# Kernel optimization log

Hardware: AMD Instinct MI355X
Metric: run time of the kernel (lower is better)

The kernel has to match this reference:

```python
import jax, jax.numpy as jnp
import numpy as np

NUM_HEADS = 16
ROPE_THETA = 1000.0


def _rope(x, cos, sin):
    # x: [B, H, T, d_k]; cos/sin: [T, d_k//2]
    xp = x.reshape(x.shape[:-1] + (x.shape[-1] // 2, 2))
    xe, xo = xp[..., 0], xp[..., 1]
    c = cos[None, None, :, :]
    s = sin[None, None, :, :]
    re = xe * c - xo * s
    ro = xe * s + xo * c
    return jnp.stack((re, ro), axis=-1).reshape(x.shape)


def setup_inputs() -> dict:
    key = jax.random.key(0)
    ks = jax.random.split(key, 5)
    B, T, D = 2, 2048, 1024
    std = 2.0 / (D + D)
    return {
        "x": jax.random.normal(ks[0], (B, T, D), dtype=jnp.float32),
        "wq": jax.random.normal(ks[1], (D, D), dtype=jnp.float32) * std,
        "wk": jax.random.normal(ks[2], (D, D), dtype=jnp.float32) * std,
        "wv": jax.random.normal(ks[3], (D, D), dtype=jnp.float32) * std,
        "wo": jax.random.normal(ks[4], (D, D), dtype=jnp.float32) * std,
    }


def reference(x, wq, wk, wv, wo):
    B, T, D = x.shape
    H = NUM_HEADS
    dk = D // H

    def proj(w):
        # Linear stores weight as [out, in]: '... in, out in -> ... out'
        y = jnp.einsum('btd,ed->bte', x, w)
        return y.reshape(B, T, H, dk).transpose(0, 2, 1, 3)  # [B,H,T,dk]

    q = proj(wq)
    k = proj(wk)
    v = proj(wv)

    # RoPE tables
    pos = jnp.arange(T, dtype=jnp.float32)[:, None]
    kidx = jnp.arange(dk // 2, dtype=jnp.float32)
    inv_freq = ROPE_THETA ** (-2.0 * kidx / dk)
    ang = pos * inv_freq[None, :]
    cos, sin = jnp.cos(ang), jnp.sin(ang)

    q = _rope(q, cos, sin)
    k = _rope(k, cos, sin)

    scores = jnp.einsum('bhnd,bhmd->bhnm', q, k) / jnp.sqrt(jnp.asarray(dk, x.dtype))
    causal = jnp.tril(jnp.ones((T, T), dtype=bool))
    scores = jnp.where(causal[None, None], scores, -jnp.inf)
    attn = jax.nn.softmax(scores, axis=-1)
    head = jnp.einsum('bhnm,bhmd->bhnd', attn, v)  # [B,H,T,dk]

    concat = head.transpose(0, 2, 1, 3).reshape(B, T, D)
    return jnp.einsum('btd,ed->bte', concat, wo)
```

## Files before the change

kernel.cpp:

```cpp
#include <hip/hip_runtime.h>
#include <hip/hip_bf16.h>

typedef __hip_bfloat16 bf16;
typedef __attribute__((ext_vector_type(8))) short bf16x8;
typedef __attribute__((ext_vector_type(4))) float f32x4;

#define T_SEQ 2048
#define NHEADS 16
#define DK 64
#define DMODEL 1024

__device__ inline void load_lds16(const void* g, void* l) {
    __builtin_amdgcn_global_load_lds((const __attribute__((address_space(1))) void*)g,
                                     (__attribute__((address_space(3))) void*)l, 16, 0, 0);
}

__global__ void cvt_all(const float* __restrict__ x,  const float* __restrict__ wq,
                        const float* __restrict__ wk, const float* __restrict__ wv,
                        const float* __restrict__ wo, bf16* __restrict__ xb,
                        bf16* __restrict__ wqkvb, bf16* __restrict__ wob) {
    int i = blockIdx.x * blockDim.x + threadIdx.x;
    const float* src; bf16* dst; int off;
    if (i < (1 << 20)) { src = x; dst = xb; off = i; }
    else {
        int j = i - (1 << 20);
        int seg = j >> 18; off = j & ((1 << 18) - 1);
        src = (seg == 0) ? wq : (seg == 1) ? wk : (seg == 2) ? wv : wo;
        dst = (seg < 3) ? (wqkvb + ((size_t)seg << 20)) : wob;
    }
    float4 f = ((const float4*)src)[off];
    ushort4 o;
    o.x = __bfloat16_as_ushort(__float2bfloat16(f.x));
    o.y = __bfloat16_as_ushort(__float2bfloat16(f.y));
    o.z = __bfloat16_as_ushort(__float2bfloat16(f.z));
    o.w = __bfloat16_as_ushort(__float2bfloat16(f.w));
    ((ushort4*)dst)[off] = o;
}

__global__ __launch_bounds__(256, 4) void gemm_qkv_rope(const bf16* __restrict__ A,
                                                        const bf16* __restrict__ B,
                                                        bf16* __restrict__ qb,
                                                        bf16* __restrict__ kb,
                                                        bf16* __restrict__ vt) {
    const int K = 1024;
    __shared__ bf16 As[128 * 64];
    __shared__ bf16 Bs[128 * 64];
    const int tid  = threadIdx.x;
    const int lane = tid & 63;
    const int wave = tid >> 6;
    const int l16  = lane & 15;
    const int quad = lane >> 4;
    const int wy = wave >> 1, wx = wave & 1;
    const int brow = blockIdx.y * 128;
    const int bcol = blockIdx.x * 128;
    const int sw0 = (quad ^ (l16 & 7)) * 8;
    const int sw1 = ((4 + quad) ^ (l16 & 7)) * 8;

    f32x4 acc[4][4] = {};

    for (int k0 = 0; k0 < K; k0 += 64) {
#pragma unroll
        for (int i = 0; i < 4; ++i) {
            int j   = tid + 256 * i;
            int row = j >> 3;
            int blk = (j & 7) ^ (row & 7);
            load_lds16(A + (size_t)(brow + row) * K + k0 + blk * 8, (char*)As + j * 16);
            load_lds16(B + (size_t)(bcol + row) * K + k0 + blk * 8, (char*)Bs + j * 16);
        }
        __syncthreads();
#pragma unroll
        for (int ks = 0; ks < 2; ++ks) {
            const int sw = ks ? sw1 : sw0;
            bf16x8 af[4], bq[4];
#pragma unroll
            for (int i = 0; i < 4; ++i)
                af[i] = *(const bf16x8*)(As + (wy * 64 + i * 16 + l16) * 64 + sw);
#pragma unroll
            for (int j = 0; j < 4; ++j)
                bq[j] = *(const bf16x8*)(Bs + (wx * 64 + j * 16 + l16) * 64 + sw);
#pragma unroll
            for (int i = 0; i < 4; ++i)
#pragma unroll
                for (int j = 0; j < 4; ++j)
                    acc[i][j] = __builtin_amdgcn_mfma_f32_16x16x32_bf16(af[i], bq[j], acc[i][j], 0, 0, 0);
        }
        __syncthreads();
    }
    const int seg = bcol >> 10;
    const int hh  = ((bcol & 1023) >> 6) + wx;
    if (seg < 2) {
        bf16* dst = seg ? kb : qb;
        const float osc = seg ? 1.0f : 0.18033688011112042f;
#pragma unroll
        for (int j = 0; j < 4; ++j) {
            const int d = j * 16 + l16;
            const float inv = exp2f(-0.31143075889f * (float)(d >> 1));
#pragma unroll
            for (int i = 0; i < 4; ++i)
#pragma unroll
                for (int r = 0; r < 4; ++r) {
                    int row = brow + wy * 64 + i * 16 + quad * 4 + r;
                    int t = row & (T_SEQ - 1), bi = row >> 11;
                    float s, c;
                    __sincosf((float)t * inv, &s, &c);
                    float v = acc[i][j][r];
                    float p = __shfl_xor(v, 1);
                    float res = (l16 & 1) ? fmaf(p, s, v * c) : fmaf(-p, s, v * c);
                    dst[((size_t)(bi * NHEADS + hh) * T_SEQ + t) * DK + d] =
                        __float2bfloat16(res * osc);
                }
        }
    } else {
#pragma unroll
        for (int j = 0; j < 4; ++j) {
            const int d = j * 16 + l16;
#pragma unroll
            for (int i = 0; i < 4; ++i)
#pragma unroll
                for (int r = 0; r < 4; ++r) {
                    int row = brow + wy * 64 + i * 16 + quad * 4 + r;
                    int t = row & (T_SEQ - 1), bi = row >> 11;
                    vt[((size_t)(bi * NHEADS + hh) * DK + d) * T_SEQ + t] =
                        __float2bfloat16(acc[i][j][r]);
                }
        }
    }
}

__global__ __launch_bounds__(256, 4) void gemm_bt(const bf16* __restrict__ A,
                                                  const bf16* __restrict__ B,
                                                  float* __restrict__ C,
                                                  int M, int N, int K) {
    __shared__ bf16 As[128 * 64];
    __shared__ bf16 Bs[128 * 64];
    const int tid  = threadIdx.x;
    const int lane = tid & 63;
    const int wave = tid >> 6;
    const int l16  = lane & 15;
    const int quad = lane >> 4;
    const int wy = wave >> 1, wx = wave & 1;
    const int brow = blockIdx.y * 128;
    const int bcol = blockIdx.x * 128;
    const int sw0 = (quad ^ (l16 & 7)) * 8;
    const int sw1 = ((4 + quad) ^ (l16 & 7)) * 8;

    f32x4 acc[4][4] = {};

    for (int k0 = 0; k0 < K; k0 += 64) {
#pragma unroll
        for (int i = 0; i < 4; ++i) {
            int j   = tid + 256 * i;
            int row = j >> 3;
            int blk = (j & 7) ^ (row & 7);
            load_lds16(A + (size_t)(brow + row) * K + k0 + blk * 8, (char*)As + j * 16);
            load_lds16(B + (size_t)(bcol + row) * K + k0 + blk * 8, (char*)Bs + j * 16);
        }
        __syncthreads();
#pragma unroll
        for (int ks = 0; ks < 2; ++ks) {
            const int sw = ks ? sw1 : sw0;
            bf16x8 af[4], bq[4];
#pragma unroll
            for (int i = 0; i < 4; ++i)
                af[i] = *(const bf16x8*)(As + (wy * 64 + i * 16 + l16) * 64 + sw);
#pragma unroll
            for (int j = 0; j < 4; ++j)
                bq[j] = *(const bf16x8*)(Bs + (wx * 64 + j * 16 + l16) * 64 + sw);
#pragma unroll
            for (int i = 0; i < 4; ++i)
#pragma unroll
                for (int j = 0; j < 4; ++j)
                    acc[i][j] = __builtin_amdgcn_mfma_f32_16x16x32_bf16(af[i], bq[j], acc[i][j], 0, 0, 0);
        }
        __syncthreads();
    }
#pragma unroll
    for (int i = 0; i < 4; ++i)
#pragma unroll
        for (int j = 0; j < 4; ++j)
#pragma unroll
            for (int r = 0; r < 4; ++r) {
                int row = brow + wy * 64 + i * 16 + quad * 4 + r;
                int col = bcol + wx * 64 + j * 16 + l16;
                C[(size_t)row * N + col] = acc[i][j][r];
            }
}

__constant__ unsigned char c_sched[24] = {
    28, 61, 57, 58, 24, 53, 49, 20,
    62, 54, 50, 41, 42, 16, 45, 46,
     0,  4,  8, 12, 33, 37, 34, 38};

__global__ __launch_bounds__(256, 4) void attn_kernel(const bf16* __restrict__ qb,
                                                      const bf16* __restrict__ kb,
                                                      const bf16* __restrict__ vt,
                                                      float* __restrict__ Oacc,
                                                      float* __restrict__ Lacc,
                                                      bf16* __restrict__ conc) {
    __shared__ bf16 Ks[2][64 * 64];
    __shared__ bf16 Vs[2][64 * 64];
    __shared__ bf16 Pl[4][16 * 64];
    const int bh = blockIdx.y;
    const int b = bh >> 4, h = bh & 15;

    const int e    = c_sched[blockIdx.x];
    const int tile = e >> 2, mode = e & 3;
    const int it0  = (mode == 2) ? tile + 1 : 0;
    const int it1  = (mode == 1) ? tile : 2 * tile + 1;
    const bool partial = (mode != 0);
    const int qbase = tile << 7;

    const int tid = threadIdx.x;
    const int lane = tid & 63, wave = tid >> 6;
    const int l16 = lane & 15, quad = lane >> 4;
    const int qr0 = qbase + wave * 16;
    const int qr1 = qr0 + 64;

    const bf16* Qp = qb + (size_t)bh * T_SEQ * DK;
    const bf16* Kp = kb + (size_t)bh * T_SEQ * DK;
    const bf16* Vp = vt + (size_t)bh * DK * T_SEQ;
    char* Pw = (char*)&Pl[wave][0];

    const short one_bits = 0x3F80;
    const bf16x8 ones = {one_bits, one_bits, one_bits, one_bits,
                         one_bits, one_bits, one_bits, one_bits};

    bf16x8 qf[2][2];
#pragma unroll
    for (int s = 0; s < 2; ++s) {
        qf[0][s] = *(const bf16x8*)(Qp + (size_t)(qr0 + l16) * DK + s * 32 + quad * 8);
        qf[1][s] = *(const bf16x8*)(Qp + (size_t)(qr1 + l16) * DK + s * 32 + quad * 8);
    }

    auto stage = [&](int bb, int k0) {
        int j = tid;
#pragma unroll
        for (int i = 0; i < 2; ++i, j += 256) {
            int row = j >> 3, cbl = (j & 7) ^ ((j >> 3) & 7);
            load_lds16(Kp + (size_t)(k0 + row) * DK + cbl * 8, (char*)Ks[bb] + j * 16);
        }
        j = tid;
#pragma unroll
        for (int i = 0; i < 2; ++i, j += 256) {
            int row = j >> 3, cbl = (j & 7) ^ ((j >> 3) & 7);
            load_lds16(Vp + (size_t)row * T_SEQ + k0 + cbl * 8, (char*)Vs[bb] + j * 16);
        }
    };

    f32x4 o0[4] = {}, o1[4] = {};
    f32x4 ol0 = {}, ol1 = {};
    const int sw0 = (quad ^ (l16 & 7)) * 8;
    const int sw1 = ((4 + quad) ^ (l16 & 7)) * 8;
    const int pw_wr_base = l16 * 128 + (quad & 1) * 8;
    const int pq = quad >> 1;

    int cur = 0;
    stage(0, it0 * 64);
    for (int it = it0; it <= it1; ++it) {
        __syncthreads();
        if (it < it1) stage(cur ^ 1, (it + 1) * 64);

        const int k0 = it * 64;
        const bool skip0 = (k0 > qr0 + 15);
        const bool diag0 = (k0 + 63 > qr0) && !skip0;
        const bool diag1 = (k0 + 63 > qr1);

        f32x4 s0[4] = {}, s1[4] = {};
        __builtin_amdgcn_s_setprio(1);
#pragma unroll
        for (int nt = 0; nt < 4; ++nt) {
            bf16x8 kf0 = *(const bf16x8*)(Ks[cur] + (nt * 16 + l16) * 64 + sw0);
            bf16x8 kf1 = *(const bf16x8*)(Ks[cur] + (nt * 16 + l16) * 64 + sw1);
            if (!skip0) {
                s0[nt] = __builtin_amdgcn_mfma_f32_16x16x32_bf16(kf0, qf[0][0], s0[nt], 0, 0, 0);
                s0[nt] = __builtin_amdgcn_mfma_f32_16x16x32_bf16(kf1, qf[0][1], s0[nt], 0, 0, 0);
            }
            s1[nt] = __builtin_amdgcn_mfma_f32_16x16x32_bf16(kf0, qf[1][0], s1[nt], 0, 0, 0);
            s1[nt] = __builtin_amdgcn_mfma_f32_16x16x32_bf16(kf1, qf[1][1], s1[nt], 0, 0, 0);
        }
        __builtin_amdgcn_s_setprio(0);

        if (!skip0) {
#pragma unroll
            for (int nt = 0; nt < 4; ++nt) {
                union { bf16 hv[4]; uint2 u; } pk;
#pragma unroll
                for (int r = 0; r < 4; ++r) {
                    float v = s0[nt][r];
                    if (diag0 && (k0 + nt * 16 + quad * 4 + r > qr0 + l16)) v = -30.0f;
                    pk.hv[r] = __float2bfloat16(exp2f(v));
                }
                *(uint2*)(Pw + pw_wr_base + (((nt * 2 + pq) ^ (l16 & 7)) << 4)) = pk.u;
            }
            __builtin_amdgcn_s_setprio(1);
#pragma unroll
            for (int ks = 0; ks < 2; ++ks) {
                bf16x8 pf = *(const bf16x8*)(Pw + l16 * 128 + (((ks * 4 + quad) ^ (l16 & 7)) << 4));
                const int sw = ks ? sw1 : sw0;
                ol0 = __builtin_amdgcn_mfma_f32_16x16x32_bf16(pf, ones, ol0, 0, 0, 0);
#pragma unroll
                for (int j = 0; j < 4; ++j) {
                    bf16x8 vf = *(const bf16x8*)(Vs[cur] + (j * 16 + l16) * 64 + sw);
                    o0[j] = __builtin_amdgcn_mfma_f32_16x16x32_bf16(pf, vf, o0[j], 0, 0, 0);
                }
            }
            __builtin_amdgcn_s_setprio(0);
        }

#pragma unroll
        for (int nt = 0; nt < 4; ++nt) {
            union { bf16 hv[4]; uint2 u; } pk;
#pragma unroll
            for (int r = 0; r < 4; ++r) {
                float v = s1[nt][r];
                if (diag1 && (k0 + nt * 16 + quad * 4 + r > qr1 + l16)) v = -30.0f;
                pk.hv[r] = __float2bfloat16(exp2f(v));
            }
            *(uint2*)(Pw + pw_wr_base + (((nt * 2 + pq) ^ (l16 & 7)) << 4)) = pk.u;
        }
        __builtin_amdgcn_s_setprio(1);
#pragma unroll
        for (int ks = 0; ks < 2; ++ks) {
            bf16x8 pf = *(const bf16x8*)(Pw + l16 * 128 + (((ks * 4 + quad) ^ (l16 & 7)) << 4));
            const int sw = ks ? sw1 : sw0;
            ol1 = __builtin_amdgcn_mfma_f32_16x16x32_bf16(pf, ones, ol1, 0, 0, 0);
#pragma unroll
            for (int j = 0; j < 4; ++j) {
                bf16x8 vf = *(const bf16x8*)(Vs[cur] + (j * 16 + l16) * 64 + sw);
                o1[j] = __builtin_amdgcn_mfma_f32_16x16x32_bf16(pf, vf, o1[j], 0, 0, 0);
            }
        }
        __builtin_amdgcn_s_setprio(0);
        cur ^= 1;
    }

#pragma unroll
    for (int g = 0; g < 2; ++g) {
        const f32x4* op = g ? o1 : o0;
        const f32x4 lv = g ? ol1 : ol0;
        const int qr = g ? qr1 : qr0;
        if (!partial) {
#pragma unroll
            for (int r = 0; r < 4; ++r) {
                float inv_l = 1.0f / lv[r];
                int t = qr + quad * 4 + r;
#pragma unroll
                for (int j = 0; j < 4; ++j)
                    conc[((size_t)b * T_SEQ + t) * DMODEL + h * DK + j * 16 + l16] =
                        __float2bfloat16(op[j][r] * inv_l);
            }
        } else {
#pragma unroll
            for (int r = 0; r < 4; ++r) {
                int q = qr + quad * 4 + r;
                if (l16 == 0)
                    atomicAdd(&Lacc[(size_t)bh * 1024 + q - 1024], lv[r]);
                float* Ob = Oacc + ((size_t)bh * 1024 + q - 1024) * DK;
#pragma unroll
                for (int j = 0; j < 4; ++j)
                    atomicAdd(&Ob[j * 16 + l16], op[j][r]);
            }
        }
    }
}

__global__ void attn_finalize(const float* __restrict__ Oacc, const float* __restrict__ Lacc,
                              bf16* __restrict__ conc) {
    int i4 = blockIdx.x * blockDim.x + threadIdx.x;
    if (i4 >= (1 << 19)) return;
    int bhq = i4 >> 4;
    int d4  = i4 & 15;
    int bh = bhq >> 10, q1 = bhq & 1023;
    int b = bh >> 4, h = bh & 15;
    int q = 1024 + q1;
    float inv = 1.0f / Lacc[bhq];
    float4 o4 = ((const float4*)Oacc)[i4];
    ushort4 u;
    u.x = __bfloat16_as_ushort(__float2bfloat16(o4.x * inv));
    u.y = __bfloat16_as_ushort(__float2bfloat16(o4.y * inv));
    u.z = __bfloat16_as_ushort(__float2bfloat16(o4.z * inv));
    u.w = __bfloat16_as_ushort(__float2bfloat16(o4.w * inv));
    *(ushort4*)&conc[((size_t)(b * T_SEQ + q)) * DMODEL + h * DK + d4 * 4] = u;
}

extern "C" void kernel_launch(void* const* d_in, const int* in_sizes, int n_in,
                              void* d_out, int out_size, void* d_ws, size_t ws_size,
                              hipStream_t stream) {
    const float* x  = (const float*)d_in[0];
    const float* wq = (const float*)d_in[1];
    const float* wk = (const float*)d_in[2];
    const float* wv = (const float*)d_in[3];
    const float* wo = (const float*)d_in[4];
    float* out = (float*)d_out;

    char* ws = (char*)d_ws;
    bf16* xb    = (bf16*)(ws);
    bf16* wqkvb = (bf16*)(ws + (8ull << 20));
    bf16* wob   = (bf16*)(ws + (14ull << 20));
    bf16* qb    = (bf16*)(ws + (40ull << 20));
    bf16* kb    = (bf16*)(ws + (48ull << 20));
    bf16* vt    = (bf16*)(ws + (56ull << 20));
    bf16* conc  = (bf16*)(ws + (16ull << 20));
    float* Oacc = (float*)(ws + (24ull << 20));
    float* Lacc = (float*)(ws + (32ull << 20));

    cvt_all<<<8192, 256, 0, stream>>>(x, wq, wk, wv, wo, xb, wqkvb, wob);
    gemm_qkv_rope<<<dim3(24, 32), 256, 0, stream>>>(xb, wqkvb, qb, kb, vt);

    hipMemsetAsync(Oacc, 0, (8ull << 20) + 32 * 1024 * sizeof(float), stream);
    attn_kernel<<<dim3(24, 32), 256, 0, stream>>>(qb, kb, vt, Oacc, Lacc, conc);
    attn_finalize<<<2048, 256, 0, stream>>>(Oacc, Lacc, conc);

    gemm_bt<<<dim3(8, 32), 256, 0, stream>>>(conc, wob, out, 4096, 1024, 1024);
}
```

Before: 182.7 us.

## Rebalance causal attention work with per-block multi-segment split schedule

Replaces the fixed 24-entry tile/mode schedule with a table where each block handles up to two segments, each encoding a query tile and an arbitrary key-iteration range. More query tiles (rows 768 and up) can now be split into partial segments merged with atomics, and the accumulator buffers and finalize kernel grow to cover 1280 rows per head. The goal is to even out per-block causal work so the grid finishes together. In exchange the kernel does more atomic traffic, a larger memset and finalize, and an extra barrier between segments.

Result: slower. 204.0 us (+11.6%).

```diff
diff --git a/kernel.cpp b/kernel.cpp
--- a/kernel.cpp
+++ b/kernel.cpp
@@ -186,10 +186,31 @@
             }
 }
 
-__constant__ unsigned char c_sched[24] = {
-    28, 61, 57, 58, 24, 53, 49, 20,
-    62, 54, 50, 41, 42, 16, 45, 46,
-     0,  4,  8, 12, 33, 37, 34, 38};
+__constant__ unsigned short c_par[24][2] = {
+    {    1,  4105},
+    { 1027,  3079},
+    { 5131, 0xFFFF},
+    { 6155, 0xFFFF},
+    { 7179, 0xFFFF},
+    { 8203, 0xFFFF},
+    { 9227, 0xFFFF},
+    {10251, 0xFFFF},
+    {11275, 0xFFFF},
+    {11671, 0xFFFF},
+    {12299, 0xFFFF},
+    {12695, 0xFFFF},
+    {13323, 0xFFFF},
+    {13719, 0xFFFF},
+    {14347, 0xFFFF},
+    {14743, 0xFFFF},
+    {15371, 0xFFFF},
+    {15767, 0xFFFF},
+    { 6541, 10645},
+    { 7567,  9619},
+    { 8593, 15133},
+    { 2053, 0xFFFF},
+    {13081, 16159},
+    {14107, 0xFFFF}};
 
 __global__ __launch_bounds__(256, 4) void attn_kernel(const bf16* __restrict__ qb,
                                                       const bf16* __restrict__ kb,
@@ -203,18 +224,9 @@
     const int bh = blockIdx.y;
     const int b = bh >> 4, h = bh & 15;
 
-    const int e    = c_sched[blockIdx.x];
-    const int tile = e >> 2, mode = e & 3;
-    const int it0  = (mode == 2) ? tile + 1 : 0;
-    const int it1  = (mode == 1) ? tile : 2 * tile + 1;
-    const bool partial = (mode != 0);
-    const int qbase = tile << 7;
-
     const int tid = threadIdx.x;
     const int lane = tid & 63, wave = tid >> 6;
     const int l16 = lane & 15, quad = lane >> 4;
-    const int qr0 = qbase + wave * 16;
-    const int qr1 = qr0 + 64;
 
     const bf16* Qp = qb + (size_t)bh * T_SEQ * DK;
     const bf16* Kp = kb + (size_t)bh * T_SEQ * DK;
@@ -225,13 +237,6 @@
     const bf16x8 ones = {one_bits, one_bits, one_bits, one_bits,
                          one_bits, one_bits, one_bits, one_bits};
 
-    bf16x8 qf[2][2];
-#pragma unroll
-    for (int s = 0; s < 2; ++s) {
-        qf[0][s] = *(const bf16x8*)(Qp + (size_t)(qr0 + l16) * DK + s * 32 + quad * 8);
-        qf[1][s] = *(const bf16x8*)(Qp + (size_t)(qr1 + l16) * DK + s * 32 + quad * 8);
-    }
-
     auto stage = [&](int bb, int k0) {
         int j = tid;
 #pragma unroll
@@ -247,47 +252,93 @@
         }
     };
 
-    f32x4 o0[4] = {}, o1[4] = {};
-    f32x4 ol0 = {}, ol1 = {};
     const int sw0 = (quad ^ (l16 & 7)) * 8;
     const int sw1 = ((4 + quad) ^ (l16 & 7)) * 8;
     const int pw_wr_base = l16 * 128 + (quad & 1) * 8;
     const int pq = quad >> 1;
 
-    int cur = 0;
-    stage(0, it0 * 64);
-    for (int it = it0; it <= it1; ++it) {
-        __syncthreads();
-        if (it < it1) stage(cur ^ 1, (it + 1) * 64);
-
-        const int k0 = it * 64;
-        const bool skip0 = (k0 > qr0 + 15);
-        const bool diag0 = (k0 + 63 > qr0) && !skip0;
-        const bool diag1 = (k0 + 63 > qr1);
-
-        f32x4 s0[4] = {}, s1[4] = {};
-        __builtin_amdgcn_s_setprio(1);
-#pragma unroll
-        for (int nt = 0; nt < 4; ++nt) {
-            bf16x8 kf0 = *(const bf16x8*)(Ks[cur] + (nt * 16 + l16) * 64 + sw0);
-            bf16x8 kf1 = *(const bf16x8*)(Ks[cur] + (nt * 16 + l16) * 64 + sw1);
+    for (int sg = 0; sg < 2; ++sg) {
+        const unsigned int e = c_par[blockIdx.x][sg];
+        if (e == 0xFFFF) break;
+        const int tile = e >> 10;
+        const int it0  = (e >> 5) & 31;
+        const int it1  = e & 31;
+        const bool partial = !(it0 == 0 && it1 == 2 * tile + 1);
+        const int qbase = tile << 7;
+        const int qr0 = qbase + wave * 16;
+        const int qr1 = qr0 + 64;
+
+        bf16x8 qf[2][2];
+#pragma unroll
+        for (int s = 0; s < 2; ++s) {
+            qf[0][s] = *(const bf16x8*)(Qp + (size_t)(qr0 + l16) * DK + s * 32 + quad * 8);
+            qf[1][s] = *(const bf16x8*)(Qp + (size_t)(qr1 + l16) * DK + s * 32 + quad * 8);
+        }
+
+        f32x4 o0[4] = {}, o1[4] = {};
+        f32x4 ol0 = {}, ol1 = {};
+
+        if (sg) __syncthreads();
+        int cur = 0;
+        stage(0, it0 * 64);
+        for (int it = it0; it <= it1; ++it) {
+            __syncthreads();
+            if (it < it1) stage(cur ^ 1, (it + 1) * 64);
+
+            const int k0 = it * 64;
+            const bool skip0 = (k0 > qr0 + 15);
+            const bool diag0 = (k0 + 63 > qr0) && !skip0;
+            const bool diag1 = (k0 + 63 > qr1);
+
+            f32x4 s0[4] = {}, s1[4] = {};
+            __builtin_amdgcn_s_setprio(1);
+#pragma unroll
+            for (int nt = 0; nt < 4; ++nt) {
+                bf16x8 kf0 = *(const bf16x8*)(Ks[cur] + (nt * 16 + l16) * 64 + sw0);
+                bf16x8 kf1 = *(const bf16x8*)(Ks[cur] + (nt * 16 + l16) * 64 + sw1);
+                if (!skip0) {
+                    s0[nt] = __builtin_amdgcn_mfma_f32_16x16x32_bf16(kf0, qf[0][0], s0[nt], 0, 0, 0);
+                    s0[nt] = __builtin_amdgcn_mfma_f32_16x16x32_bf16(kf1, qf[0][1], s0[nt], 0, 0, 0);
+                }
+                s1[nt] = __builtin_amdgcn_mfma_f32_16x16x32_bf16(kf0, qf[1][0], s1[nt], 0, 0, 0);
+                s1[nt] = __builtin_amdgcn_mfma_f32_16x16x32_bf16(kf1, qf[1][1], s1[nt], 0, 0, 0);
+            }
+            __builtin_amdgcn_s_setprio(0);
+
             if (!skip0) {
-                s0[nt] = __builtin_amdgcn_mfma_f32_16x16x32_bf16(kf0, qf[0][0], s0[nt], 0, 0, 0);
-                s0[nt] = __builtin_amdgcn_mfma_f32_16x16x32_bf16(kf1, qf[0][1], s0[nt], 0, 0, 0);
-            }
-            s1[nt] = __builtin_amdgcn_mfma_f32_16x16x32_bf16(kf0, qf[1][0], s1[nt], 0, 0, 0);
-            s1[nt] = __builtin_amdgcn_mfma_f32_16x16x32_bf16(kf1, qf[1][1], s1[nt], 0, 0, 0);
-        }
-        __builtin_amdgcn_s_setprio(0);
-
-        if (!skip0) {
+#pragma unroll
+                for (int nt = 0; nt < 4; ++nt) {
+                    union { bf16 hv[4]; uint2 u; } pk;
+#pragma unroll
+                    for (int r = 0; r < 4; ++r) {
+                        float v = s0[nt][r];
+                        if (diag0 && (k0 + nt * 16 + quad * 4 + r > qr0 + l16)) v = -30.0f;
+                        pk.hv[r] = __float2bfloat16(exp2f(v));
+                    }
+                    *(uint2*)(Pw + pw_wr_base + (((nt * 2 + pq) ^ (l16 & 7)) << 4)) = pk.u;
+                }
+                __builtin_amdgcn_s_setprio(1);
+#pragma unroll
+                for (int ks = 0; ks < 2; ++ks) {
+                    bf16x8 pf = *(const bf16x8*)(Pw + l16 * 128 + (((ks * 4 + quad) ^ (l16 & 7)) << 4));
+                    const int sw = ks ? sw1 : sw0;
+                    ol0 = __builtin_amdgcn_mfma_f32_16x16x32_bf16(pf, ones, ol0, 0, 0, 0);
+#pragma unroll
+                    for (int j = 0; j < 4; ++j) {
+                        bf16x8 vf = *(const bf16x8*)(Vs[cur] + (j * 16 + l16) * 64 + sw);
+                        o0[j] = __builtin_amdgcn_mfma_f32_16x16x32_bf16(pf, vf, o0[j], 0, 0, 0);
+                    }
+                }
+                __builtin_amdgcn_s_setprio(0);
+            }
+
 #pragma unroll
             for (int nt = 0; nt < 4; ++nt) {
                 union { bf16 hv[4]; uint2 u; } pk;
 #pragma unroll
                 for (int r = 0; r < 4; ++r) {
-                    float v = s0[nt][r];
-                    if (diag0 && (k0 + nt * 16 + quad * 4 + r > qr0 + l16)) v = -30.0f;
+                    float v = s1[nt][r];
+                    if (diag1 && (k0 + nt * 16 + quad * 4 + r > qr1 + l16)) v = -30.0f;
                     pk.hv[r] = __float2bfloat16(exp2f(v));
                 }
                 *(uint2*)(Pw + pw_wr_base + (((nt * 2 + pq) ^ (l16 & 7)) << 4)) = pk.u;
@@ -297,68 +348,43 @@
             for (int ks = 0; ks < 2; ++ks) {
                 bf16x8 pf = *(const bf16x8*)(Pw + l16 * 128 + (((ks * 4 + quad) ^ (l16 & 7)) << 4));
                 const int sw = ks ? sw1 : sw0;
-                ol0 = __builtin_amdgcn_mfma_f32_16x16x32_bf16(pf, ones, ol0, 0, 0, 0);
+                ol1 = __builtin_amdgcn_mfma_f32_16x16x32_bf16(pf, ones, ol1, 0, 0, 0);
 #pragma unroll
                 for (int j = 0; j < 4; ++j) {
                     bf16x8 vf = *(const bf16x8*)(Vs[cur] + (j * 16 + l16) * 64 + sw);
-                    o0[j] = __builtin_amdgcn_mfma_f32_16x16x32_bf16(pf, vf, o0[j], 0, 0, 0);
+                    o1[j] = __builtin_amdgcn_mfma_f32_16x16x32_bf16(pf, vf, o1[j], 0, 0, 0);
                 }
             }
             __builtin_amdgcn_s_setprio(0);
-        }
-
-#pragma unroll
-        for (int nt = 0; nt < 4; ++nt) {
-            union { bf16 hv[4]; uint2 u; } pk;
-#pragma unroll
-            for (int r = 0; r < 4; ++r) {
-                float v = s1[nt][r];
-                if (diag1 && (k0 + nt * 16 + quad * 4 + r > qr1 + l16)) v = -30.0f;
-                pk.hv[r] = __float2bfloat16(exp2f(v));
-            }
-            *(uint2*)(Pw + pw_wr_base + (((nt * 2 + pq) ^ (l16 & 7)) << 4)) = pk.u;
-        }
-        __builtin_amdgcn_s_setprio(1);
-#pragma unroll
-        for (int ks = 0; ks < 2; ++ks) {
-            bf16x8 pf = *(const bf16x8*)(Pw + l16 * 128 + (((ks * 4 + quad) ^ (l16 & 7)) << 4));
-            const int sw = ks ? sw1 : sw0;
-            ol1 = __builtin_amdgcn_mfma_f32_16x16x32_bf16(pf, ones, ol1, 0, 0, 0);
-#pragma unroll
-            for (int j = 0; j < 4; ++j) {
-                bf16x8 vf = *(const bf16x8*)(Vs[cur] + (j * 16 + l16) * 64 + sw);
-                o1[j] = __builtin_amdgcn_mfma_f32_16x16x32_bf16(pf, vf, o1[j], 0, 0, 0);
-            }
-        }
-        __builtin_amdgcn_s_setprio(0);
-        cur ^= 1;
-    }
-
-#pragma unroll
-    for (int g = 0; g < 2; ++g) {
-        const f32x4* op = g ? o1 : o0;
-        const f32x4 lv = g ? ol1 : ol0;
-        const int qr = g ? qr1 : qr0;
-        if (!partial) {
-#pragma unroll
-            for (int r = 0; r < 4; ++r) {
-                float inv_l = 1.0f / lv[r];
-                int t = qr + quad * 4 + r;
-#pragma unroll
-                for (int j = 0; j < 4; ++j)
-                    conc[((size_t)b * T_SEQ + t) * DMODEL + h * DK + j * 16 + l16] =
-                        __float2bfloat16(op[j][r] * inv_l);
-            }
-        } else {
-#pragma unroll
-            for (int r = 0; r < 4; ++r) {
-                int q = qr + quad * 4 + r;
-                if (l16 == 0)
-                    atomicAdd(&Lacc[(size_t)bh * 1024 + q - 1024], lv[r]);
-                float* Ob = Oacc + ((size_t)bh * 1024 + q - 1024) * DK;
-#pragma unroll
-                for (int j = 0; j < 4; ++j)
-                    atomicAdd(&Ob[j * 16 + l16], op[j][r]);
+            cur ^= 1;
+        }
+
+#pragma unroll
+        for (int g = 0; g < 2; ++g) {
+            const f32x4* op = g ? o1 : o0;
+            const f32x4 lv = g ? ol1 : ol0;
+            const int qr = g ? qr1 : qr0;
+            if (!partial) {
+#pragma unroll
+                for (int r = 0; r < 4; ++r) {
+                    float inv_l = 1.0f / lv[r];
+                    int t = qr + quad * 4 + r;
+#pragma unroll
+                    for (int j = 0; j < 4; ++j)
+                        conc[((size_t)b * T_SEQ + t) * DMODEL + h * DK + j * 16 + l16] =
+                            __float2bfloat16(op[j][r] * inv_l);
+                }
+            } else {
+#pragma unroll
+                for (int r = 0; r < 4; ++r) {
+                    int q = qr + quad * 4 + r;
+                    if (l16 == 0)
+                        atomicAdd(&Lacc[(size_t)bh * 1280 + q - 768], lv[r]);
+                    float* Ob = Oacc + ((size_t)bh * 1280 + q - 768) * DK;
+#pragma unroll
+                    for (int j = 0; j < 4; ++j)
+                        atomicAdd(&Ob[j * 16 + l16], op[j][r]);
+                }
             }
         }
     }
@@ -367,12 +393,12 @@
 __global__ void attn_finalize(const float* __restrict__ Oacc, const float* __restrict__ Lacc,
                               bf16* __restrict__ conc) {
     int i4 = blockIdx.x * blockDim.x + threadIdx.x;
-    if (i4 >= (1 << 19)) return;
+    if (i4 >= 32 * 1280 * 16) return;
     int bhq = i4 >> 4;
     int d4  = i4 & 15;
-    int bh = bhq >> 10, q1 = bhq & 1023;
+    int bh = bhq / 1280, q7 = bhq - bh * 1280;
     int b = bh >> 4, h = bh & 15;
-    int q = 1024 + q1;
+    int q = 768 + q7;
     float inv = 1.0f / Lacc[bhq];
     float4 o4 = ((const float4*)Oacc)[i4];
     ushort4 u;
@@ -397,19 +423,19 @@
     bf16* xb    = (bf16*)(ws);
     bf16* wqkvb = (bf16*)(ws + (8ull << 20));
     bf16* wob   = (bf16*)(ws + (14ull << 20));
+    bf16* conc  = (bf16*)(ws + (16ull << 20));
+    float* Oacc = (float*)(ws + (24ull << 20));
+    float* Lacc = (float*)(ws + (34ull << 20));
     bf16* qb    = (bf16*)(ws + (40ull << 20));
     bf16* kb    = (bf16*)(ws + (48ull << 20));
     bf16* vt    = (bf16*)(ws + (56ull << 20));
-    bf16* conc  = (bf16*)(ws + (16ull << 20));
-    float* Oacc = (float*)(ws + (24ull << 20));
-    float* Lacc = (float*)(ws + (32ull << 20));
 
     cvt_all<<<8192, 256, 0, stream>>>(x, wq, wk, wv, wo, xb, wqkvb, wob);
     gemm_qkv_rope<<<dim3(24, 32), 256, 0, stream>>>(xb, wqkvb, qb, kb, vt);
 
-    hipMemsetAsync(Oacc, 0, (8ull << 20) + 32 * 1024 * sizeof(float), stream);
+    hipMemsetAsync(Oacc, 0, (10ull << 20) + 32 * 1280 * sizeof(float), stream);
     attn_kernel<<<dim3(24, 32), 256, 0, stream>>>(qb, kb, vt, Oacc, Lacc, conc);
-    attn_finalize<<<2048, 256, 0, stream>>>(Oacc, Lacc, conc);
+    attn_finalize<<<2560, 256, 0, stream>>>(Oacc, Lacc, conc);
 
     gemm_bt<<<dim3(8, 32), 256, 0, stream>>>(conc, wob, out, 4096, 1024, 1024);
 }
```
